# Kernel optimization log

Hardware: AMD Instinct MI355X
Metric: run time of the kernel (lower is better)

Reference implementation:

```python
import jax, jax.numpy as jnp
import numpy as np

BATCH, SEQ, CH, ORDER = 4, 8192, 512, 64


def setup_inputs() -> dict:
    key = jax.random.key(0)
    k1, k2, k3 = jax.random.split(key, 3)
    x = jax.random.normal(k1, (BATCH, SEQ, CH), dtype=jnp.float32)
    # RTF parameters: small init so the denominator polynomial 1 + sum a_i z^-i
    # stays well-conditioned (stable transfer function), as in the FSSM init.
    A = 0.01 * jax.random.normal(k2, (CH, ORDER), dtype=jnp.float32)
    B = 0.01 * jax.random.normal(k3, (CH, ORDER), dtype=jnp.float32)
    h0 = jnp.zeros((1,), dtype=jnp.float32)
    return {"x": x, "A": A, "B": B, "h0": h0}


def _rtf_kernel(A, B, L):
    # Evaluate H(z) = b(z)/a(z) at the L roots of unity, then irfft -> impulse response.
    C = A.shape[0]
    a = jnp.concatenate([jnp.ones((C, 1), A.dtype), A], axis=-1)  # (C, N+1), leading coeff 1
    a_f = jnp.fft.rfft(a, n=L, axis=-1)                           # (C, L//2+1)
    b_f = jnp.fft.rfft(B, n=L, axis=-1)
    return jnp.fft.irfft(b_f / a_f, n=L, axis=-1)                 # (C, L)


def reference(x, A, B, h0):
    Bt, L, C = x.shape
    K = _rtf_kernel(A, B, L)                                      # (C, L)
    n_fft = 2 * L                                                 # causal (linear) convolution
    x_f = jnp.fft.rfft(x, n=n_fft, axis=1)                        # (B, n_fft//2+1, C)
    k_f = jnp.fft.rfft(K, n=n_fft, axis=-1).T[None]               # (1, n_fft//2+1, C)
    h1 = jnp.fft.irfft(x_f * k_f, n=n_fft, axis=1)[:, :L]         # (B, L, C)
    y1 = h1 + h0 * x
    return jax.nn.gelu(y1)
```

## Files before the change

kernel.cpp:

```cpp
#include <hip/hip_runtime.h>
#include <stdint.h>

#define NBATCH 4
#define LSEQ   8192
#define CH     512
#define ORDER  64
#define KTAP   256
#define NW     9

typedef _Float16 half8 __attribute__((ext_vector_type(8)));
typedef __fp16   fp16x2 __attribute__((ext_vector_type(2)));
typedef float    f32x4 __attribute__((ext_vector_type(4)));

#define AFRAG_HALFS  ((size_t)CH * NW * 64 * 8)
#define WS_NEED      (AFRAG_HALFS * 2)

#define XROWB 1584
#define SMEMB (16 * XROWB)
#define LOWB  1040
#define PAIRS 392

__device__ __forceinline__ uint32_t pkrtz(float lo, float hi) {
    fp16x2 v = __builtin_amdgcn_cvt_pkrtz(lo, hi);
    return __builtin_bit_cast(uint32_t, v);
}

__global__ __launch_bounds__(256) void rtf_afrag(const float* __restrict__ A,
                                                 const float* __restrict__ B,
                                                 const float* __restrict__ h0,
                                                 _Float16* __restrict__ afr) {
    __shared__ float Ksh[4][KTAP];
    const int wv = threadIdx.x >> 6, lane = threadIdx.x & 63;
    const int c  = blockIdx.x * 4 + wv;
    const float a  = A[c * ORDER + lane];
    const float bc = B[c * ORDER + lane];
    const float h0v = h0[0];
    float s = 0.0f;
    for (int t = 0; t < KTAP; ++t) {
        const float s1 = __shfl(s, 0);
        const float bt = (t < ORDER) ? __shfl(bc, t) : 0.0f;
        const float y  = bt + s1;
        float su = __shfl_down(s, 1);
        if (lane == ORDER - 1) su = 0.0f;
        s = su - a * y;
        if (lane == 0) Ksh[wv][t] = (t == 0) ? (y + h0v) : y;
    }
    __syncthreads();
    const int i = lane & 15, g = lane >> 4;
    for (int w = 0; w < NW; ++w) {
        half8 hv;
#pragma unroll
        for (int e = 0; e < 8; ++e) {
            const int t = 32 * w + 15 + i - 8 * g - e;
            hv[e] = (_Float16)((t >= 0 && t < KTAP) ? Ksh[wv][t] : 0.0f);
        }
        *reinterpret_cast<half8*>(afr + ((size_t)(c * NW + w) * 64 + lane) * 8) = hv;
    }
}

__global__ __launch_bounds__(256) void fir_direct(const float* __restrict__ x,
                                                  const _Float16* __restrict__ afr,
                                                  float* __restrict__ out) {
    __shared__ __align__(16) char smem[SMEMB];
    const int gid     = blockIdx.x;
    const int logical = (gid & 7) * 256 + (gid >> 3);
    const int chgrp   = logical >> 6;
    const int bb      = (logical >> 4) & 3;
    const int tg      = logical & 15;
    const int n0      = tg * 512;
    const int c0      = chgrp * 16;

    {
        const int q  = threadIdx.x & 3;
        const int pr = threadIdx.x >> 2;
        const float* xsrc = x + (size_t)bb * LSEQ * CH + c0 + q * 4;
        f32x4 L0[7], L1[7];
#pragma unroll
        for (int i = 0; i < 7; ++i) {
            const int p = pr + 64 * i;
            f32x4 z = {0.f, 0.f, 0.f, 0.f};
            L0[i] = z; L1[i] = z;
            if (p < PAIRS) {
                const int r0 = n0 - 271 + 2 * p;
                if ((unsigned)r0 < LSEQ)       L0[i] = *reinterpret_cast<const f32x4*>(xsrc + (size_t)r0 * CH);
                if ((unsigned)(r0 + 1) < LSEQ) L1[i] = *reinterpret_cast<const f32x4*>(xsrc + (size_t)(r0 + 1) * CH);
            }
        }
#pragma unroll
        for (int i = 0; i < 7; ++i) {
            const int p = pr + 64 * i;
            if (p < PAIRS) {
                char* wb = smem + (size_t)(4 * q) * XROWB + 4 * p;
                *reinterpret_cast<uint32_t*>(wb + 0 * XROWB) = pkrtz(L0[i][0], L1[i][0]);
                *reinterpret_cast<uint32_t*>(wb + 1 * XROWB) = pkrtz(L0[i][1], L1[i][1]);
                *reinterpret_cast<uint32_t*>(wb + 2 * XROWB) = pkrtz(L0[i][2], L1[i][2]);
                *reinterpret_cast<uint32_t*>(wb + 3 * XROWB) = pkrtz(L0[i][3], L1[i][3]);
            }
        }
    }
    __syncthreads();

    const int wid = threadIdx.x >> 6, lane = threadIdx.x & 63;
    const int j = lane & 15, g = lane >> 4;
    const int c0w = c0 + wid * 4;
    const _Float16* af = afr + (size_t)lane * 8;

    f32x4 acc[2][4];
#pragma unroll
    for (int ti = 0; ti < 2; ++ti)
#pragma unroll
        for (int q = 0; q < 4; ++q) acc[ti][q] = (f32x4){0.f, 0.f, 0.f, 0.f};

#pragma unroll
    for (int w = 0; w < NW; ++w) {
        half8 a[4];
#pragma unroll
        for (int q = 0; q < 4; ++q)
            a[q] = *reinterpret_cast<const half8*>(af + (size_t)((c0w + q) * NW + w) * 512);
        const int idx0 = 16 * j + 8 * g - 32 * w + 256;
#pragma unroll
        for (int ti = 0; ti < 2; ++ti) {
#pragma unroll
            for (int q = 0; q < 4; ++q) {
                const half8 bv = *reinterpret_cast<const half8*>(
                    smem + (size_t)(wid * 4 + q) * XROWB + 2 * (idx0 + 256 * ti));
                acc[ti][q] = __builtin_amdgcn_mfma_f32_16x16x32_f16(a[q], bv, acc[ti][q], 0, 0, 0);
            }
        }
    }

    const int cq  = threadIdx.x & 3;
    const int nr0 = threadIdx.x >> 2;
#pragma unroll
    for (int ti = 0; ti < 2; ++ti) {
        __syncthreads();
#pragma unroll
        for (int q = 0; q < 4; ++q) {
            f32x4 o;
#pragma unroll
            for (int r = 0; r < 4; ++r) {
                const float y  = acc[ti][q][r];
                const float wv = fmaf(y * y, 0.14270963f, 1.5957691f);
                const float e  = __expf(y * wv);
                o[r] = y - y * __builtin_amdgcn_rcpf(e + 1.0f);
            }
            *reinterpret_cast<f32x4*>(smem + (size_t)(wid * 4 + q) * LOWB
                                      + 4 * (16 * j + 4 * g)) = o;
        }
        __syncthreads();
        float* obp = out + ((size_t)bb * LSEQ + n0 + ti * 256) * CH + c0 + 4 * cq;
#pragma unroll
        for (int it = 0; it < 4; ++it) {
            const int n = nr0 + 64 * it;
            f32x4 o;
            o[0] = *reinterpret_cast<const float*>(smem + (size_t)(4 * cq + 0) * LOWB + 4 * n);
            o[1] = *reinterpret_cast<const float*>(smem + (size_t)(4 * cq + 1) * LOWB + 4 * n);
            o[2] = *reinterpret_cast<const float*>(smem + (size_t)(4 * cq + 2) * LOWB + 4 * n);
            o[3] = *reinterpret_cast<const float*>(smem + (size_t)(4 * cq + 3) * LOWB + 4 * n);
            *reinterpret_cast<f32x4*>(obp + (size_t)n * CH) = o;
        }
    }
}

#define RINGF 32
#define CPBF  256
__global__ __launch_bounds__(ORDER) void rtf_impulse_fb(const float* __restrict__ A,
                                                        const float* __restrict__ B,
                                                        const float* __restrict__ h0,
                                                        float* __restrict__ kt4) {
    const int c = blockIdx.x, lane = threadIdx.x;
    const float a = A[c * ORDER + lane], bc = B[c * ORDER + lane], h0v = h0[0];
    float s = 0.0f;
    for (int t = 0; t < KTAP; ++t) {
        const float s1 = __shfl(s, 0);
        const float bt = (t < ORDER) ? __shfl(bc, t) : 0.0f;
        const float y  = bt + s1;
        float su = __shfl_down(s, 1);
        if (lane == ORDER - 1) su = 0.0f;
        s = su - a * y;
        if (lane == 0) kt4[((size_t)(t >> 2) * CH + c) * 4 + (t & 3)] = (t == 0) ? (y + h0v) : y;
    }
}
__global__ __launch_bounds__(CPBF) void fir_gelu_fb(const float* __restrict__ x,
                                                    const float* __restrict__ kt4,
                                                    float* __restrict__ out) {
    const int h = blockIdx.x;
    const int logical = ((h & 7) << 8) | (h >> 3);
    const int tile = logical & 255, sl = logical >> 8;
    const int cb = sl & 1, b = sl >> 1;
    const int c = cb * CPBF + threadIdx.x;
    const int n0 = tile * RINGF;
    const float* xb = x + (size_t)b * LSEQ * CH + c;
    const float4* kt4v = (const float4*)kt4;
    float acc[RINGF]; float ring[RINGF]; float px[2][8]; float kbuf[2][8];
#pragma unroll
    for (int r = 0; r < RINGF; ++r) acc[r] = 0.0f;
#pragma unroll
    for (int i = 0; i < RINGF; ++i) ring[i] = xb[(size_t)(n0 + i) * CH];
    {
        const float4 ka = kt4v[(size_t)0 * CH + c];
        const float4 kb = kt4v[(size_t)1 * CH + c];
        kbuf[0][0] = ka.x; kbuf[0][1] = ka.y; kbuf[0][2] = ka.z; kbuf[0][3] = ka.w;
        kbuf[0][4] = kb.x; kbuf[0][5] = kb.y; kbuf[0][6] = kb.z; kbuf[0][7] = kb.w;
#pragma unroll
        for (int g2 = 0; g2 < 8; ++g2) {
            const int m = n0 - 1 - g2;
            px[0][g2] = (m >= 0) ? xb[(size_t)m * CH] : 0.0f;
        }
    }
    for (int tb = 0; tb < KTAP; tb += RINGF) {
#pragma unroll
        for (int qq = 0; qq < 4; ++qq) {
            const int cur = qq & 1, nxt = cur ^ 1;
            const int tn = tb + 8 * (qq + 1);
            if (tn < KTAP) {
                const float4 ka = kt4v[(size_t)(tn >> 2) * CH + c];
                const float4 kb = kt4v[(size_t)((tn >> 2) + 1) * CH + c];
                kbuf[nxt][0] = ka.x; kbuf[nxt][1] = ka.y; kbuf[nxt][2] = ka.z; kbuf[nxt][3] = ka.w;
                kbuf[nxt][4] = kb.x; kbuf[nxt][5] = kb.y; kbuf[nxt][6] = kb.z; kbuf[nxt][7] = kb.w;
#pragma unroll
                for (int g2 = 0; g2 < 8; ++g2) {
                    const int m = n0 - tn - 1 - g2;
                    px[nxt][g2] = (m >= 0) ? xb[(size_t)m * CH] : 0.0f;
                }
            }
#pragma unroll
            for (int g2 = 0; g2 < 8; ++g2) {
                const int tq = 8 * qq + g2;
                const float kv = kbuf[cur][g2];
#pragma unroll
                for (int r = 0; r < RINGF; ++r)
                    acc[r] = fmaf(kv, ring[(r - tq) & (RINGF - 1)], acc[r]);
                ring[(RINGF - 1 - tq) & (RINGF - 1)] = px[cur][g2];
            }
        }
    }
    float* ob = out + ((size_t)b * LSEQ + n0) * CH + c;
#pragma unroll
    for (int r = 0; r < RINGF; ++r) {
        const float y = acc[r];
        const float wv = fmaf(y * y, 0.14270963f, 1.5957691f);
        const float e = __expf(y * wv);
        ob[(size_t)r * CH] = y - y * __builtin_amdgcn_rcpf(e + 1.0f);
    }
}

extern "C" void kernel_launch(void* const* d_in, const int* in_sizes, int n_in,
                              void* d_out, int out_size, void* d_ws, size_t ws_size,
                              hipStream_t stream) {
    const float* x  = (const float*)d_in[0];
    const float* A  = (const float*)d_in[1];
    const float* B  = (const float*)d_in[2];
    const float* h0 = (const float*)d_in[3];
    float* out = (float*)d_out;

    if (ws_size >= WS_NEED) {
        _Float16* afr = (_Float16*)d_ws;
        rtf_afrag<<<dim3(CH / 4), dim3(256), 0, stream>>>(A, B, h0, afr);
        fir_direct<<<dim3(2048), dim3(256), 0, stream>>>(x, afr, out);
    } else {
        float* kt4 = (float*)d_ws;
        rtf_impulse_fb<<<dim3(CH), dim3(ORDER), 0, stream>>>(A, B, h0, kt4);
        fir_gelu_fb<<<dim3((LSEQ / RINGF) * (CH / CPBF) * NBATCH), dim3(CPBF), 0, stream>>>(x, kt4, out);
    }
}
```

Before: 66.22 us.

## Make FIR kernel persistent over four time tiles with register-prefetched input

The FIR conv+GELU kernel now processes four consecutive 512-sample tiles per block instead of one, launching 512 blocks instead of 2048. The next tile's x rows are loaded into registers while the current tile's MFMAs and GELU epilogue run, then written to LDS. Kernel fragments are also software-prefetched one window ahead. The aim is to hide global load latency and amortize block startup. The cost is fewer blocks, which may underfill the GPU's CUs, plus higher register pressure from the prefetch buffers under a 2-blocks-per-CU launch bound.

Measured after the change: 71.86 us. 8.5% more time.

```diff
diff --git a/kernel.cpp b/kernel.cpp
--- a/kernel.cpp
+++ b/kernel.cpp
@@ -17,8 +17,8 @@
 
 #define XROWB 1584
 #define SMEMB (16 * XROWB)
-#define LOWB  1040
 #define PAIRS 392
+#define TPB   4
 
 __device__ __forceinline__ uint32_t pkrtz(float lo, float hi) {
     fp16x2 v = __builtin_amdgcn_cvt_pkrtz(lo, hi);
@@ -58,108 +58,141 @@
     }
 }
 
-__global__ __launch_bounds__(256) void fir_direct(const float* __restrict__ x,
-                                                  const _Float16* __restrict__ afr,
-                                                  float* __restrict__ out) {
-    __shared__ __align__(16) char smem[SMEMB];
+__global__ __launch_bounds__(256, 2) void fir_pipe(const float* __restrict__ x,
+                                                   const _Float16* __restrict__ afr,
+                                                   float* __restrict__ out) {
+    __shared__ __align__(16) char  xs[SMEMB];
+    __shared__ float lout[16][260];
     const int gid     = blockIdx.x;
-    const int logical = (gid & 7) * 256 + (gid >> 3);
-    const int chgrp   = logical >> 6;
-    const int bb      = (logical >> 4) & 3;
-    const int tg      = logical & 15;
-    const int n0      = tg * 512;
+    const int logical = (gid & 7) * 64 + (gid >> 3);
+    const int chgrp   = logical >> 4;
+    const int bb      = (logical >> 2) & 3;
+    const int qt      = logical & 3;
+    const int nbase   = qt * (TPB * 512);
     const int c0      = chgrp * 16;
 
-    {
-        const int q  = threadIdx.x & 3;
-        const int pr = threadIdx.x >> 2;
-        const float* xsrc = x + (size_t)bb * LSEQ * CH + c0 + q * 4;
-        f32x4 L0[7], L1[7];
-#pragma unroll
-        for (int i = 0; i < 7; ++i) {
-            const int p = pr + 64 * i;
-            f32x4 z = {0.f, 0.f, 0.f, 0.f};
-            L0[i] = z; L1[i] = z;
-            if (p < PAIRS) {
-                const int r0 = n0 - 271 + 2 * p;
-                if ((unsigned)r0 < LSEQ)       L0[i] = *reinterpret_cast<const f32x4*>(xsrc + (size_t)r0 * CH);
-                if ((unsigned)(r0 + 1) < LSEQ) L1[i] = *reinterpret_cast<const f32x4*>(xsrc + (size_t)(r0 + 1) * CH);
-            }
-        }
-#pragma unroll
-        for (int i = 0; i < 7; ++i) {
-            const int p = pr + 64 * i;
-            if (p < PAIRS) {
-                char* wb = smem + (size_t)(4 * q) * XROWB + 4 * p;
-                *reinterpret_cast<uint32_t*>(wb + 0 * XROWB) = pkrtz(L0[i][0], L1[i][0]);
-                *reinterpret_cast<uint32_t*>(wb + 1 * XROWB) = pkrtz(L0[i][1], L1[i][1]);
-                *reinterpret_cast<uint32_t*>(wb + 2 * XROWB) = pkrtz(L0[i][2], L1[i][2]);
-                *reinterpret_cast<uint32_t*>(wb + 3 * XROWB) = pkrtz(L0[i][3], L1[i][3]);
-            }
-        }
-    }
+    const int q  = threadIdx.x & 3;
+    const int pr = threadIdx.x >> 2;
+    const float* xsrc = x + (size_t)bb * LSEQ * CH + c0 + q * 4;
+
+    f32x4 L0[7], L1[7];
+
+#define LOAD_TILE(N0K)                                                        \
+    {                                                                         \
+        _Pragma("unroll")                                                     \
+        for (int i = 0; i < 7; ++i) {                                         \
+            const int p = pr + 64 * i;                                        \
+            f32x4 z = {0.f, 0.f, 0.f, 0.f};                                   \
+            L0[i] = z; L1[i] = z;                                             \
+            if (p < PAIRS) {                                                  \
+                const int r0 = (N0K) - 271 + 2 * p;                           \
+                if ((unsigned)r0 < LSEQ)                                      \
+                    L0[i] = *reinterpret_cast<const f32x4*>(xsrc + (size_t)r0 * CH); \
+                if ((unsigned)(r0 + 1) < LSEQ)                                \
+                    L1[i] = *reinterpret_cast<const f32x4*>(xsrc + (size_t)(r0 + 1) * CH); \
+            }                                                                 \
+        }                                                                     \
+    }
+
+#define WRITE_XS()                                                            \
+    {                                                                         \
+        _Pragma("unroll")                                                     \
+        for (int i = 0; i < 7; ++i) {                                         \
+            const int p = pr + 64 * i;                                        \
+            if (p < PAIRS) {                                                  \
+                char* wb = xs + (size_t)(4 * q) * XROWB + 4 * p;              \
+                *reinterpret_cast<uint32_t*>(wb + 0 * XROWB) = pkrtz(L0[i][0], L1[i][0]); \
+                *reinterpret_cast<uint32_t*>(wb + 1 * XROWB) = pkrtz(L0[i][1], L1[i][1]); \
+                *reinterpret_cast<uint32_t*>(wb + 2 * XROWB) = pkrtz(L0[i][2], L1[i][2]); \
+                *reinterpret_cast<uint32_t*>(wb + 3 * XROWB) = pkrtz(L0[i][3], L1[i][3]); \
+            }                                                                 \
+        }                                                                     \
+    }
+
+    LOAD_TILE(nbase);
+    WRITE_XS();
+    LOAD_TILE(nbase + 512);
     __syncthreads();
 
     const int wid = threadIdx.x >> 6, lane = threadIdx.x & 63;
     const int j = lane & 15, g = lane >> 4;
     const int c0w = c0 + wid * 4;
     const _Float16* af = afr + (size_t)lane * 8;
-
-    f32x4 acc[2][4];
-#pragma unroll
-    for (int ti = 0; ti < 2; ++ti)
-#pragma unroll
-        for (int q = 0; q < 4; ++q) acc[ti][q] = (f32x4){0.f, 0.f, 0.f, 0.f};
-
-#pragma unroll
-    for (int w = 0; w < NW; ++w) {
-        half8 a[4];
-#pragma unroll
-        for (int q = 0; q < 4; ++q)
-            a[q] = *reinterpret_cast<const half8*>(af + (size_t)((c0w + q) * NW + w) * 512);
-        const int idx0 = 16 * j + 8 * g - 32 * w + 256;
-#pragma unroll
-        for (int ti = 0; ti < 2; ++ti) {
-#pragma unroll
-            for (int q = 0; q < 4; ++q) {
-                const half8 bv = *reinterpret_cast<const half8*>(
-                    smem + (size_t)(wid * 4 + q) * XROWB + 2 * (idx0 + 256 * ti));
-                acc[ti][q] = __builtin_amdgcn_mfma_f32_16x16x32_f16(a[q], bv, acc[ti][q], 0, 0, 0);
-            }
-        }
-    }
-
     const int cq  = threadIdx.x & 3;
     const int nr0 = threadIdx.x >> 2;
-#pragma unroll
-    for (int ti = 0; ti < 2; ++ti) {
-        __syncthreads();
-#pragma unroll
-        for (int q = 0; q < 4; ++q) {
-            f32x4 o;
-#pragma unroll
-            for (int r = 0; r < 4; ++r) {
-                const float y  = acc[ti][q][r];
-                const float wv = fmaf(y * y, 0.14270963f, 1.5957691f);
-                const float e  = __expf(y * wv);
-                o[r] = y - y * __builtin_amdgcn_rcpf(e + 1.0f);
-            }
-            *reinterpret_cast<f32x4*>(smem + (size_t)(wid * 4 + q) * LOWB
-                                      + 4 * (16 * j + 4 * g)) = o;
-        }
-        __syncthreads();
-        float* obp = out + ((size_t)bb * LSEQ + n0 + ti * 256) * CH + c0 + 4 * cq;
-#pragma unroll
-        for (int it = 0; it < 4; ++it) {
-            const int n = nr0 + 64 * it;
-            f32x4 o;
-            o[0] = *reinterpret_cast<const float*>(smem + (size_t)(4 * cq + 0) * LOWB + 4 * n);
-            o[1] = *reinterpret_cast<const float*>(smem + (size_t)(4 * cq + 1) * LOWB + 4 * n);
-            o[2] = *reinterpret_cast<const float*>(smem + (size_t)(4 * cq + 2) * LOWB + 4 * n);
-            o[3] = *reinterpret_cast<const float*>(smem + (size_t)(4 * cq + 3) * LOWB + 4 * n);
-            *reinterpret_cast<f32x4*>(obp + (size_t)n * CH) = o;
-        }
-    }
+
+#pragma unroll 1
+    for (int k = 0; k < TPB; ++k) {
+        const int n0 = nbase + 512 * k;
+
+        f32x4 acc[2][4];
+#pragma unroll
+        for (int ti = 0; ti < 2; ++ti)
+#pragma unroll
+            for (int qq = 0; qq < 4; ++qq) acc[ti][qq] = (f32x4){0.f, 0.f, 0.f, 0.f};
+
+        half8 a_cur[4], a_nxt[4];
+#pragma unroll
+        for (int qq = 0; qq < 4; ++qq)
+            a_cur[qq] = *reinterpret_cast<const half8*>(af + (size_t)((c0w + qq) * NW + 0) * 512);
+#pragma unroll
+        for (int w = 0; w < NW; ++w) {
+            if (w < NW - 1) {
+#pragma unroll
+                for (int qq = 0; qq < 4; ++qq)
+                    a_nxt[qq] = *reinterpret_cast<const half8*>(af + (size_t)((c0w + qq) * NW + (w + 1)) * 512);
+            }
+            const int idx0 = 16 * j + 8 * g - 32 * w + 256;
+#pragma unroll
+            for (int ti = 0; ti < 2; ++ti) {
+#pragma unroll
+                for (int qq = 0; qq < 4; ++qq) {
+                    const half8 bv = *reinterpret_cast<const half8*>(
+                        xs + (size_t)(wid * 4 + qq) * XROWB + 2 * (idx0 + 256 * ti));
+                    acc[ti][qq] = __builtin_amdgcn_mfma_f32_16x16x32_f16(a_cur[qq], bv, acc[ti][qq], 0, 0, 0);
+                }
+            }
+#pragma unroll
+            for (int qq = 0; qq < 4; ++qq) a_cur[qq] = a_nxt[qq];
+        }
+
+#pragma unroll
+        for (int ti = 0; ti < 2; ++ti) {
+            __syncthreads();
+#pragma unroll
+            for (int qq = 0; qq < 4; ++qq) {
+                f32x4 o;
+#pragma unroll
+                for (int r = 0; r < 4; ++r) {
+                    const float y  = acc[ti][qq][r];
+                    const float wv = fmaf(y * y, 0.14270963f, 1.5957691f);
+                    const float e  = __expf(y * wv);
+                    o[r] = y - y * __builtin_amdgcn_rcpf(e + 1.0f);
+                }
+                *reinterpret_cast<f32x4*>(&lout[wid * 4 + qq][16 * j + 4 * g]) = o;
+            }
+            __syncthreads();
+            float* obp = out + ((size_t)bb * LSEQ + n0 + ti * 256) * CH + c0 + 4 * cq;
+#pragma unroll
+            for (int it = 0; it < 4; ++it) {
+                const int n = nr0 + 64 * it;
+                f32x4 o;
+                o[0] = lout[4 * cq + 0][n];
+                o[1] = lout[4 * cq + 1][n];
+                o[2] = lout[4 * cq + 2][n];
+                o[3] = lout[4 * cq + 3][n];
+                *reinterpret_cast<f32x4*>(obp + (size_t)n * CH) = o;
+            }
+        }
+
+        if (k < TPB - 1) {
+            WRITE_XS();
+            if (k < TPB - 2) LOAD_TILE(nbase + 512 * (k + 2));
+            __syncthreads();
+        }
+    }
+#undef LOAD_TILE
+#undef WRITE_XS
 }
 
 #define RINGF 32
@@ -257,7 +290,7 @@
     if (ws_size >= WS_NEED) {
         _Float16* afr = (_Float16*)d_ws;
         rtf_afrag<<<dim3(CH / 4), dim3(256), 0, stream>>>(A, B, h0, afr);
-        fir_direct<<<dim3(2048), dim3(256), 0, stream>>>(x, afr, out);
+        fir_pipe<<<dim3(512), dim3(256), 0, stream>>>(x, afr, out);
     } else {
         float* kt4 = (float*)d_ws;
         rtf_impulse_fb<<<dim3(CH), dim3(ORDER), 0, stream>>>(A, B, h0, kt4);
```
